# Optimization experiments

Measured on AMD Instinct MI355X. Metric: run time of the kernel, lower is better.

## Reference

```python
import jax, jax.numpy as jnp
import numpy as np

B, D, H, W, T, C = 2, 16, 16, 16, 16, 96
NH = 4                      # num_heads
WS = (4, 4, 4, 4)           # window size
SS = (2, 2, 2, 2)           # shift size
EPS = 1e-5
HIDDEN = 4 * C


def _compute_mask():
    # Standard Swin shifted-window attention mask, extended to 4D.
    img = np.zeros((D, H, W, T), np.float32)
    sl = [[slice(0, -WS[i]), slice(-WS[i], -SS[i]), slice(-SS[i], None)] for i in range(4)]
    cnt = 0
    for a in sl[0]:
        for b in sl[1]:
            for c in sl[2]:
                for d in sl[3]:
                    img[a, b, c, d] = cnt
                    cnt += 1
    x = img.reshape(D // WS[0], WS[0], H // WS[1], WS[1], W // WS[2], WS[2], T // WS[3], WS[3])
    x = x.transpose(0, 2, 4, 6, 1, 3, 5, 7).reshape(-1, WS[0] * WS[1] * WS[2] * WS[3])
    diff = x[:, None, :] - x[:, :, None]
    return np.where(diff != 0, np.float32(-100.0), np.float32(0.0))


def setup_inputs() -> dict:
    key = jax.random.key(0)
    ks = jax.random.split(key, 6)
    w = lambda k, shape: jax.random.normal(k, shape, jnp.float32) * 0.02
    return {
        'x': jax.random.normal(ks[0], (B, D, H, W, T, C), jnp.float32),
        'mask_matrix': jnp.asarray(_compute_mask()),
        'norm1_g': jnp.ones((C,), jnp.float32), 'norm1_b': jnp.zeros((C,), jnp.float32),
        'qkv_w': w(ks[1], (3 * C, C)), 'qkv_b': jnp.zeros((3 * C,), jnp.float32),
        'proj_w': w(ks[2], (C, C)), 'proj_b': jnp.zeros((C,), jnp.float32),
        'norm2_g': jnp.ones((C,), jnp.float32), 'norm2_b': jnp.zeros((C,), jnp.float32),
        'fc1_w': w(ks[3], (HIDDEN, C)), 'fc1_b': jnp.zeros((HIDDEN,), jnp.float32),
        'fc2_w': w(ks[4], (C, HIDDEN)), 'fc2_b': jnp.zeros((C,), jnp.float32),
    }


def _ln(x, g, b):
    mu = jnp.mean(x, -1, keepdims=True)
    var = jnp.var(x, -1, keepdims=True)
    return (x - mu) * jax.lax.rsqrt(var + EPS) * g + b


def _partition(x):
    # (B, D, H, W, T, C) -> (B*nw, N, C)
    b, c = x.shape[0], x.shape[-1]
    x = x.reshape(b, D // WS[0], WS[0], H // WS[1], WS[1], W // WS[2], WS[2], T // WS[3], WS[3], c)
    x = x.transpose(0, 1, 3, 5, 7, 2, 4, 6, 8, 9)
    return x.reshape(-1, WS[0] * WS[1] * WS[2] * WS[3], c)


def _reverse(win, b):
    c = win.shape[-1]
    x = win.reshape(b, D // WS[0], H // WS[1], W // WS[2], T // WS[3], WS[0], WS[1], WS[2], WS[3], c)
    x = x.transpose(0, 1, 5, 2, 6, 3, 7, 4, 8, 9)
    return x.reshape(b, D, H, W, T, c)


def reference(x, mask_matrix, norm1_g, norm1_b, qkv_w, qkv_b, proj_w, proj_b,
              norm2_g, norm2_b, fc1_w, fc1_b, fc2_w, fc2_b):
    b, c = x.shape[0], x.shape[-1]
    hd = c // NH
    scale = hd ** -0.5
    shortcut = x
    # norm -> (no pad needed: dims divisible by window) -> cyclic shift
    xn = _ln(x, norm1_g, norm1_b)
    xs = jnp.roll(xn, shift=(-SS[0], -SS[1], -SS[2], -SS[3]), axis=(1, 2, 3, 4))
    win = _partition(xs)                              # (B_, N, C)
    B_, N, _ = win.shape
    qkv = (win @ qkv_w.T + qkv_b).reshape(B_, N, 3, NH, hd).transpose(2, 0, 3, 1, 4)
    q, k, v = qkv[0] * scale, qkv[1], qkv[2]          # (B_, NH, N, hd)
    attn = jnp.einsum('bhid,bhjd->bhij', q, k)        # (B_, NH, N, N)
    nw = mask_matrix.shape[0]
    attn = attn.reshape(B_ // nw, nw, NH, N, N) + mask_matrix[None, :, None]
    attn = jax.nn.softmax(attn.reshape(B_, NH, N, N), axis=-1)
    out = jnp.einsum('bhij,bhjd->bhid', attn, v)
    out = out.transpose(0, 2, 1, 3).reshape(B_, N, c)
    out = out @ proj_w.T + proj_b
    xr = _reverse(out, b)
    xr = jnp.roll(xr, shift=SS, axis=(1, 2, 3, 4))    # reverse cyclic shift
    x = shortcut + xr
    # MLP block
    h = _ln(x, norm2_g, norm2_b)
    h = jax.nn.gelu(h @ fc1_w.T + fc1_b, approximate=False)
    return x + (h @ fc2_w.T + fc2_b)
```

## Files before the change

### kernel.cpp

```cpp
#include <hip/hip_runtime.h>

#define TOK   131072
#define BWIN  512

typedef __attribute__((ext_vector_type(8))) short bf16x8;
typedef __attribute__((ext_vector_type(4))) short bf16x4;
typedef __attribute__((ext_vector_type(4))) float f32x4;

__device__ __forceinline__ unsigned short f2us(float f) {
  union { float f; unsigned int i; } x; x.f = f;
  return (unsigned short)((x.i + 0x7fffu + ((x.i >> 16) & 1u)) >> 16);
}
__device__ __forceinline__ unsigned cvtpk(float lo, float hi) {
  unsigned r;
  asm("v_cvt_pk_bf16_f32 %0, %1, %2" : "=v"(r) : "v"(lo), "v"(hi));
  return r;
}
union U8 { uint2 u; bf16x4 v; };

#define IW1   0
#define IW2   36864
#define IQKV  73728
#define IPROJ 104448
#define IMG_SHORTS 113664

__global__ __launch_bounds__(256) void k_prepw(
    const float* __restrict__ fc1_w, const float* __restrict__ fc2_w,
    const float* __restrict__ qkv_w, const float* __restrict__ proj_w,
    unsigned short* __restrict__ img) {
  int i = blockIdx.x * 256 + threadIdx.x;
  const int l = (i >> 3) & 63, j = i & 7;
  const int quad = l >> 4, l15 = l & 15;
  float v = 0.f;
  if (i < 36864) {
    int f = i >> 9; int nc = f / 18, rem = f - nc * 18;
    int ks = rem / 6, nt = rem - ks * 6;
    v = fc1_w[(size_t)(nc * 96 + nt * 16 + l15) * 96 + ks * 32 + quad * 8 + j];
  } else if (i < 73728) {
    int f = (i - 36864) >> 9; int nc = f / 18, rem = f - nc * 18;
    int ks = rem / 6, nt = rem - ks * 6;
    v = fc2_w[(size_t)(nt * 16 + l15) * 384 + nc * 96 + ks * 32 + quad * 8 + j];
  } else if (i < 104448) {
    int f = (i - 73728) >> 9; int h = f / 15, rem = f - h * 15;
    int ks = rem / 5, mt = rem - ks * 5;
    int e = mt * 16 + l15;
    if (e < 72) {
      int grp = e / 24, rr = e - grp * 24;
      v = qkv_w[(size_t)(grp * 96 + h * 24 + rr) * 96 + ks * 32 + quad * 8 + j];
    }
  } else {
    int f = (i - 104448) >> 9; int ks = f / 6, nt = f - ks * 6;
    v = proj_w[(size_t)(nt * 16 + l15) * 96 + ks * 32 + quad * 8 + j];
  }
  img[i] = f2us(v);
}

__global__ __launch_bounds__(256) void k_ln1(const float* __restrict__ x,
                                             const float* __restrict__ g,
                                             const float* __restrict__ b,
                                             unsigned short* __restrict__ xn) {
  const int r = threadIdx.x >> 1, hf = threadIdx.x & 1;
  const int t = blockIdx.x * 128 + r;
  const int b_ = t >> 8, n = t & 255;
  const int batch = b_ >> 8, wi = b_ & 255;
  const int wd = (wi >> 6) & 3, wh = (wi >> 4) & 3, ww = (wi >> 2) & 3, wt = wi & 3;
  const int aa = (n >> 6) & 3, bb = (n >> 4) & 3, cc = (n >> 2) & 3, dd = n & 3;
  const int sd = (wd * 4 + aa + 2) & 15, sh = (wh * 4 + bb + 2) & 15;
  const int sw = (ww * 4 + cc + 2) & 15, st = (wt * 4 + dd + 2) & 15;
  const size_t gg = ((((size_t)(batch * 16 + sd) * 16 + sh) * 16 + sw) * 16 + st);

  const float4* base = (const float4*)(x + gg * 96 + hf * 48);
  float v[48];
  float s = 0.f, q2 = 0.f;
  #pragma unroll
  for (int j = 0; j < 12; j++) {
    float4 f = base[j];
    v[4 * j] = f.x; v[4 * j + 1] = f.y; v[4 * j + 2] = f.z; v[4 * j + 3] = f.w;
    s += f.x + f.y + f.z + f.w;
    q2 += f.x * f.x + f.y * f.y + f.z * f.z + f.w * f.w;
  }
  s += __shfl_xor(s, 1); q2 += __shfl_xor(q2, 1);
  const float mu = s * (1.f / 96.f);
  const float var = q2 * (1.f / 96.f) - mu * mu;
  const float rs = rsqrtf(fmaxf(var, 0.f) + 1e-5f);
  unsigned int* row = (unsigned int*)xn + (size_t)t * 48 + hf * 24;
  #pragma unroll
  for (int jj = 0; jj < 24; jj++) {
    int k0 = hf * 48 + 2 * jj;
    float a0 = (v[2 * jj]     - mu) * rs * g[k0]     + b[k0];
    float a1 = (v[2 * jj + 1] - mu) * rs * g[k0 + 1] + b[k0 + 1];
    row[jj] = cvtpk(a0, a1);
  }
}

__global__ __launch_bounds__(256, 2) void k_win(
    const unsigned short* __restrict__ xn,
    const unsigned short* __restrict__ img,
    const float* __restrict__ qkv_b,
    unsigned short* __restrict__ og) {
  __shared__ __align__(16) short s_k[256 * 36];
  __shared__ __align__(16) short s_vt[32 * 260];
  __shared__ unsigned char s_lb[256];

  const int tid = threadIdx.x;
  const int w = tid >> 6, l = tid & 63, quad = l >> 4, l15 = l & 15;
  const int q0 = w * 64;
  const int b_ = blockIdx.x;
  const int wi = b_ & 255;
  const int wd = (wi >> 6) & 3, wh = (wi >> 4) & 3, ww = (wi >> 2) & 3, wt = wi & 3;
  const float scale = 0.20412414523193154f;
  const f32x4 fz = {0.f, 0.f, 0.f, 0.f};

  {
    const int n = tid;
    const int aa = (n >> 6) & 3, bb = (n >> 4) & 3, cc = (n >> 2) & 3, dd = n & 3;
    const int p0 = wd * 4 + aa, p1 = wh * 4 + bb, p2 = ww * 4 + cc, p3 = wt * 4 + dd;
    const int r0 = p0 >= 14 ? 2 : (p0 >= 12 ? 1 : 0);
    const int r1 = p1 >= 14 ? 2 : (p1 >= 12 ? 1 : 0);
    const int r2 = p2 >= 14 ? 2 : (p2 >= 12 ? 1 : 0);
    const int r3 = p3 >= 14 ? 2 : (p3 >= 12 ? 1 : 0);
    s_lb[n] = (unsigned char)(((r0 * 3 + r1) * 3 + r2) * 3 + r3);
    *(uint2*)&s_k[n * 36 + 24] = make_uint2(0u, 0u);
    *(uint2*)&s_k[n * 36 + 28] = make_uint2(0u, 0u);
    unsigned int* vz = (unsigned int*)(s_vt + 24 * 260);
    for (int i = tid; i < 8 * 130; i += 256) vz[i] = 0u;
  }
  __syncthreads();

  const unsigned short* xw = xn + (size_t)b_ * 256 * 96;
  const unsigned short* wq = img + IQKV;

  for (int h = 0; h < 4; h++) {
    f32x4 acc[5][4];
    #pragma unroll
    for (int mt = 0; mt < 5; mt++)
      #pragma unroll
      for (int nt = 0; nt < 4; nt++) acc[mt][nt] = fz;
    #pragma unroll
    for (int ks = 0; ks < 3; ks++) {
      bf16x8 aw[5];
      #pragma unroll
      for (int mt = 0; mt < 5; mt++)
        aw[mt] = *(const bf16x8*)(wq + ((h * 3 + ks) * 5 + mt) * 512 + l * 8);
      #pragma unroll
      for (int nt = 0; nt < 4; nt++) {
        bf16x8 bx = *(const bf16x8*)(xw + (size_t)(q0 + nt * 16 + l15) * 96 + ks * 32 + quad * 8);
        #pragma unroll
        for (int mt = 0; mt < 5; mt++)
          acc[mt][nt] = __builtin_amdgcn_mfma_f32_16x16x32_bf16(aw[mt], bx, acc[mt][nt], 0, 0, 0);
      }
    }
    U8 qq[2][4];
    #pragma unroll
    for (int mt = 0; mt < 2; mt++) {
      const int e0 = mt * 16 + quad * 4;
      float b0 = qkv_b[h * 24 + e0],     b1 = qkv_b[h * 24 + e0 + 1];
      float b2 = qkv_b[h * 24 + e0 + 2], b3 = qkv_b[h * 24 + e0 + 3];
      #pragma unroll
      for (int nt = 0; nt < 4; nt++) {
        qq[mt][nt].u.x = cvtpk((acc[mt][nt][0] + b0) * scale, (acc[mt][nt][1] + b1) * scale);
        qq[mt][nt].u.y = cvtpk((acc[mt][nt][2] + b2) * scale, (acc[mt][nt][3] + b3) * scale);
      }
    }
    #pragma unroll
    for (int mt = 1; mt < 5; mt++) {
      const int e0 = mt * 16 + quad * 4;
      #pragma unroll
      for (int nt = 0; nt < 4; nt++) {
        const int tok = q0 + nt * 16 + l15;
        if (e0 >= 24 && e0 < 48) {
          const int e = e0 - 24;
          uint2 pk;
          pk.x = cvtpk(acc[mt][nt][0] + qkv_b[96 + h * 24 + e],
                       acc[mt][nt][1] + qkv_b[96 + h * 24 + e + 1]);
          pk.y = cvtpk(acc[mt][nt][2] + qkv_b[96 + h * 24 + e + 2],
                       acc[mt][nt][3] + qkv_b[96 + h * 24 + e + 3]);
          *(uint2*)&s_k[tok * 36 + e] = pk;
        } else if (e0 >= 48 && e0 < 72) {
          const int e = e0 - 48;
          #pragma unroll
          for (int r = 0; r < 4; r++)
            s_vt[(e + r) * 260 + tok] = (short)f2us(acc[mt][nt][r] + qkv_b[192 + h * 24 + e + r]);
        }
      }
    }
    __syncthreads();
    #pragma unroll 1
    for (int mt4 = 0; mt4 < 4; mt4++) {
      const int qt0 = q0 + mt4 * 16;
      f32x4 sc[16];
      #pragma unroll
      for (int km = 0; km < 16; km++) sc[km] = fz;
      const bf16x4 bq0 = qq[0][mt4].v, bq1 = qq[1][mt4].v;
      __builtin_amdgcn_s_setprio(1);
      #pragma unroll
      for (int km = 0; km < 16; km++) {
        bf16x4 ak0 = *(const bf16x4*)&s_k[(km * 16 + l15) * 36 + quad * 4];
        bf16x4 ak1 = *(const bf16x4*)&s_k[(km * 16 + l15) * 36 + 16 + quad * 4];
        sc[km] = __builtin_amdgcn_mfma_f32_16x16x16bf16_1k(ak0, bq0, sc[km], 0, 0, 0);
        sc[km] = __builtin_amdgcn_mfma_f32_16x16x16bf16_1k(ak1, bq1, sc[km], 0, 0, 0);
      }
      __builtin_amdgcn_s_setprio(0);
      const unsigned lq = s_lb[qt0 + l15];
      float rsum = 0.f;
      #pragma unroll
      for (int km = 0; km < 16; km++) {
        unsigned lj = *(const unsigned*)&s_lb[km * 16 + quad * 4];
        float p0 = ((lj & 255u)         == lq) ? __expf(sc[km][0]) : 0.f;
        float p1 = (((lj >> 8) & 255u)  == lq) ? __expf(sc[km][1]) : 0.f;
        float p2 = (((lj >> 16) & 255u) == lq) ? __expf(sc[km][2]) : 0.f;
        float p3 = ((lj >> 24)          == lq) ? __expf(sc[km][3]) : 0.f;
        sc[km][0] = p0; sc[km][1] = p1; sc[km][2] = p2; sc[km][3] = p3;
        rsum += (p0 + p1) + (p2 + p3);
      }
      rsum += __shfl_xor(rsum, 16, 64);
      rsum += __shfl_xor(rsum, 32, 64);
      const float inv = 1.f / rsum;
      f32x4 ov0 = fz, ov1 = fz;
      __builtin_amdgcn_s_setprio(1);
      #pragma unroll
      for (int km = 0; km < 16; km++) {
        U8 bp;
        bp.u.x = cvtpk(sc[km][0], sc[km][1]);
        bp.u.y = cvtpk(sc[km][2], sc[km][3]);
        bf16x4 av0 = *(const bf16x4*)&s_vt[l15 * 260 + km * 16 + quad * 4];
        bf16x4 av1 = *(const bf16x4*)&s_vt[(16 + l15) * 260 + km * 16 + quad * 4];
        ov0 = __builtin_amdgcn_mfma_f32_16x16x16bf16_1k(av0, bp.v, ov0, 0, 0, 0);
        ov1 = __builtin_amdgcn_mfma_f32_16x16x16bf16_1k(av1, bp.v, ov1, 0, 0, 0);
      }
      __builtin_amdgcn_s_setprio(0);
      uint2 o0, o1;
      o0.x = cvtpk(ov0[0] * inv, ov0[1] * inv);
      o0.y = cvtpk(ov0[2] * inv, ov0[3] * inv);
      o1.x = cvtpk(ov1[0] * inv, ov1[1] * inv);
      o1.y = cvtpk(ov1[2] * inv, ov1[3] * inv);
      size_t ob = ((size_t)b_ * 256 + qt0 + l15) * 96 + h * 24;
      *(uint2*)&og[ob + quad * 4] = o0;
      if (quad < 2) *(uint2*)&og[ob + 16 + quad * 4] = o1;
    }
    __syncthreads();
  }
}

__global__ __launch_bounds__(256, 2) void k_proj(
    const unsigned short* __restrict__ og, const float* __restrict__ x,
    const unsigned short* __restrict__ img,
    const float* __restrict__ proj_b, float* __restrict__ out) {
  const int tid = threadIdx.x;
  const int w = tid >> 6, l = tid & 63, quad = l >> 4, l15 = l & 15;
  const int t0 = blockIdx.x * 128;
  const f32x4 fz = {0.f, 0.f, 0.f, 0.f};

  f32x4 acc[2][6];
  #pragma unroll
  for (int m = 0; m < 2; m++)
    #pragma unroll
    for (int nt = 0; nt < 6; nt++) acc[m][nt] = fz;

  #pragma unroll
  for (int ks = 0; ks < 3; ks++) {
    bf16x8 bw[6];
    #pragma unroll
    for (int nt = 0; nt < 6; nt++)
      bw[nt] = *(const bf16x8*)(img + IPROJ + (ks * 6 + nt) * 512 + l * 8);
    #pragma unroll
    for (int m = 0; m < 2; m++) {
      bf16x8 af = *(const bf16x8*)(og + (size_t)(t0 + w * 32 + m * 16 + l15) * 96 + ks * 32 + quad * 8);
      #pragma unroll
      for (int nt = 0; nt < 6; nt++)
        acc[m][nt] = __builtin_amdgcn_mfma_f32_16x16x32_bf16(af, bw[nt], acc[m][nt], 0, 0, 0);
    }
  }

  #pragma unroll
  for (int m = 0; m < 2; m++) {
    #pragma unroll
    for (int r = 0; r < 4; r++) {
      const int T = t0 + w * 32 + m * 16 + quad * 4 + r;
      const int b_ = T >> 8, n = T & 255;
      const int batch = b_ >> 8, wi = b_ & 255;
      const int wd = (wi >> 6) & 3, wh = (wi >> 4) & 3, ww = (wi >> 2) & 3, wt = wi & 3;
      const int aa = (n >> 6) & 3, bb = (n >> 4) & 3, cc = (n >> 2) & 3, dd = n & 3;
      const int sd = (wd * 4 + aa + 2) & 15, sh = (wh * 4 + bb + 2) & 15;
      const int sw = (ww * 4 + cc + 2) & 15, st = (wt * 4 + dd + 2) & 15;
      const size_t gg = ((((size_t)(batch * 16 + sd) * 16 + sh) * 16 + sw) * 16 + st);
      #pragma unroll
      for (int nt = 0; nt < 6; nt++) {
        int c = nt * 16 + l15;
        out[gg * 96 + c] = x[gg * 96 + c] + proj_b[c] + acc[m][nt][r];
      }
    }
  }
}

__global__ __launch_bounds__(256, 3) void k_mlp(
    float* __restrict__ io,
    const float* __restrict__ n2g, const float* __restrict__ n2b,
    const unsigned short* __restrict__ img,
    const float* __restrict__ fc1_b, const float* __restrict__ fc2_b) {
  __shared__ __align__(16) short s_a[128 * 104];
  __shared__ __align__(16) short s_h[128 * 104];

  const int tid = threadIdx.x;
  const int w = tid >> 6, l = tid & 63;
  const int quad = l >> 4, l15 = l & 15;
  const size_t t0 = (size_t)blockIdx.x * 128;
  const f32x4 fz = {0.f, 0.f, 0.f, 0.f};

  {
    const int r = tid >> 1, hf = tid & 1;
    const float4* base = (const float4*)(io + (t0 + r) * 96 + hf * 48);
    float v[48];
    float s = 0.f, q = 0.f;
    #pragma unroll
    for (int j = 0; j < 12; j++) {
      float4 f = base[j];
      v[4 * j] = f.x; v[4 * j + 1] = f.y; v[4 * j + 2] = f.z; v[4 * j + 3] = f.w;
      s += f.x + f.y + f.z + f.w;
      q += f.x * f.x + f.y * f.y + f.z * f.z + f.w * f.w;
    }
    s += __shfl_xor(s, 1); q += __shfl_xor(q, 1);
    const float mu = s * (1.f / 96.f);
    const float var = q * (1.f / 96.f) - mu * mu;
    const float rs = rsqrtf(fmaxf(var, 0.f) + 1e-5f);
    unsigned int* row = (unsigned int*)&s_a[r * 104] + hf * 24;
    #pragma unroll
    for (int jj = 0; jj < 24; jj++) {
      int k0 = hf * 48 + 2 * jj;
      float lo = (v[2 * jj]     - mu) * rs * n2g[k0]     + n2b[k0];
      float hi = (v[2 * jj + 1] - mu) * rs * n2g[k0 + 1] + n2b[k0 + 1];
      row[jj] = cvtpk(lo, hi);
    }
  }

  f32x4 acc2[2][6];
  #pragma unroll
  for (int m = 0; m < 2; m++)
    #pragma unroll
    for (int i = 0; i < 6; i++) acc2[m][i] = fz;

  for (int nc = 0; nc < 4; nc++) {
    f32x4 acc1[2][6];
    #pragma unroll
    for (int m = 0; m < 2; m++)
      #pragma unroll
      for (int i = 0; i < 6; i++) acc1[m][i] = fz;
    #pragma unroll
    for (int ks = 0; ks < 3; ks++) {
      bf16x8 bw[6];
      #pragma unroll
      for (int nt = 0; nt < 6; nt++)
        bw[nt] = *(const bf16x8*)(img + IW1 + ((nc * 3 + ks) * 6 + nt) * 512 + l * 8);
      #pragma unroll
      for (int m = 0; m < 2; m++) {
        bf16x8 af = *(const bf16x8*)&s_a[(w * 32 + m * 16 + l15) * 104 + ks * 32 + quad * 8];
        #pragma unroll
        for (int nt = 0; nt < 6; nt++)
          acc1[m][nt] = __builtin_amdgcn_mfma_f32_16x16x32_bf16(af, bw[nt], acc1[m][nt], 0, 0, 0);
      }
    }
    #pragma unroll
    for (int m = 0; m < 2; m++)
      #pragma unroll
      for (int nt = 0; nt < 6; nt++) {
        int col = nt * 16 + l15;
        float bv = fc1_b[nc * 96 + col];
        #pragma unroll
        for (int r = 0; r < 4; r++) {
          float z = acc1[m][nt][r] + bv;
          float g = 0.5f * z * (1.f + erff(z * 0.70710678118654752f));
          s_h[(w * 32 + m * 16 + quad * 4 + r) * 104 + col] = (short)f2us(g);
        }
      }
    #pragma unroll
    for (int ks = 0; ks < 3; ks++) {
      bf16x8 bw[6];
      #pragma unroll
      for (int nt = 0; nt < 6; nt++)
        bw[nt] = *(const bf16x8*)(img + IW2 + ((nc * 3 + ks) * 6 + nt) * 512 + l * 8);
      #pragma unroll
      for (int m = 0; m < 2; m++) {
        bf16x8 af = *(const bf16x8*)&s_h[(w * 32 + m * 16 + l15) * 104 + ks * 32 + quad * 8];
        #pragma unroll
        for (int nt = 0; nt < 6; nt++)
          acc2[m][nt] = __builtin_amdgcn_mfma_f32_16x16x32_bf16(af, bw[nt], acc2[m][nt], 0, 0, 0);
      }
    }
  }

  #pragma unroll
  for (int m = 0; m < 2; m++)
    #pragma unroll
    for (int nt = 0; nt < 6; nt++) {
      int col = nt * 16 + l15;
      float bv = fc2_b[col];
      #pragma unroll
      for (int r = 0; r < 4; r++) {
        size_t idx = (t0 + w * 32 + m * 16 + quad * 4 + r) * 96 + col;
        io[idx] = io[idx] + acc2[m][nt][r] + bv;
      }
    }
}

extern "C" void kernel_launch(void* const* d_in, const int* in_sizes, int n_in,
                              void* d_out, int out_size, void* d_ws, size_t ws_size,
                              hipStream_t stream) {
  const float* x      = (const float*)d_in[0];
  const float* n1g    = (const float*)d_in[2];
  const float* n1b    = (const float*)d_in[3];
  const float* qkv_w  = (const float*)d_in[4];
  const float* qkv_b  = (const float*)d_in[5];
  const float* proj_w = (const float*)d_in[6];
  const float* proj_b = (const float*)d_in[7];
  const float* n2g    = (const float*)d_in[8];
  const float* n2b    = (const float*)d_in[9];
  const float* fc1_w  = (const float*)d_in[10];
  const float* fc1_b  = (const float*)d_in[11];
  const float* fc2_w  = (const float*)d_in[12];
  const float* fc2_b  = (const float*)d_in[13];
  float* out = (float*)d_out;

  char* ws = (char*)d_ws;
  unsigned short* xn  = (unsigned short*)ws;
  unsigned short* img = (unsigned short*)(ws + 25165824u);
  unsigned short* og  = (unsigned short*)(ws + 25165824u + 227328u);

  k_prepw<<<IMG_SHORTS / 256, 256, 0, stream>>>(fc1_w, fc2_w, qkv_w, proj_w, img);
  k_ln1<<<TOK / 128, 256, 0, stream>>>(x, n1g, n1b, xn);
  k_win<<<BWIN, 256, 0, stream>>>(xn, img, qkv_b, og);
  k_proj<<<TOK / 128, 256, 0, stream>>>(og, x, img, proj_b, out);
  k_mlp<<<TOK / 128, 256, 0, stream>>>(out, n2g, n2b, img, fc1_b, fc2_b);
}
```

Before: 314.8 us.

## Fuse projection, residual, LayerNorm2 and MLP into one kernel

Merges k_proj and k_mlp into a single kernel. The projection result plus residual stays in registers, LayerNorm2 is computed with cross-lane shuffles, and the MLP output is scattered straight to its final un-shifted location. This removes one fp32 write and re-read of the full 50MB intermediate plus one launch. In exchange it raises register pressure (x2, gg and pacc held across the MLP) while keeping launch bounds at 2 blocks per SM instead of 3, which may lower occupancy. The final stores are scattered rather than contiguous.

```diff
diff --git a/kernel.cpp b/kernel.cpp
--- a/kernel.cpp
+++ b/kernel.cpp
@@ -242,21 +242,33 @@
   }
 }
 
-__global__ __launch_bounds__(256, 2) void k_proj(
+__global__ __launch_bounds__(256, 2) void k_pm(
     const unsigned short* __restrict__ og, const float* __restrict__ x,
     const unsigned short* __restrict__ img,
-    const float* __restrict__ proj_b, float* __restrict__ out) {
+    const float* __restrict__ proj_b,
+    const float* __restrict__ n2g, const float* __restrict__ n2b,
+    const float* __restrict__ fc1_b, const float* __restrict__ fc2_b,
+    float* __restrict__ out) {
+  __shared__ __align__(16) short s_a[128 * 104];
+  __shared__ __align__(16) short s_h[128 * 104];
+
   const int tid = threadIdx.x;
   const int w = tid >> 6, l = tid & 63, quad = l >> 4, l15 = l & 15;
   const int t0 = blockIdx.x * 128;
   const f32x4 fz = {0.f, 0.f, 0.f, 0.f};
 
-  f32x4 acc[2][6];
+  float gn[6], bn[6], pb[6], f2[6];
+  #pragma unroll
+  for (int nt = 0; nt < 6; nt++) {
+    int c = nt * 16 + l15;
+    gn[nt] = n2g[c]; bn[nt] = n2b[c]; pb[nt] = proj_b[c]; f2[nt] = fc2_b[c];
+  }
+
+  f32x4 pacc[2][6];
   #pragma unroll
   for (int m = 0; m < 2; m++)
     #pragma unroll
-    for (int nt = 0; nt < 6; nt++) acc[m][nt] = fz;
-
+    for (int nt = 0; nt < 6; nt++) pacc[m][nt] = fz;
   #pragma unroll
   for (int ks = 0; ks < 3; ks++) {
     bf16x8 bw[6];
@@ -268,10 +280,12 @@
       bf16x8 af = *(const bf16x8*)(og + (size_t)(t0 + w * 32 + m * 16 + l15) * 96 + ks * 32 + quad * 8);
       #pragma unroll
       for (int nt = 0; nt < 6; nt++)
-        acc[m][nt] = __builtin_amdgcn_mfma_f32_16x16x32_bf16(af, bw[nt], acc[m][nt], 0, 0, 0);
-    }
-  }
-
+        pacc[m][nt] = __builtin_amdgcn_mfma_f32_16x16x32_bf16(af, bw[nt], pacc[m][nt], 0, 0, 0);
+    }
+  }
+
+  float x2[2][6][4];
+  size_t gg[2][4];
   #pragma unroll
   for (int m = 0; m < 2; m++) {
     #pragma unroll
@@ -283,53 +297,26 @@
       const int aa = (n >> 6) & 3, bb = (n >> 4) & 3, cc = (n >> 2) & 3, dd = n & 3;
       const int sd = (wd * 4 + aa + 2) & 15, sh = (wh * 4 + bb + 2) & 15;
       const int sw = (ww * 4 + cc + 2) & 15, st = (wt * 4 + dd + 2) & 15;
-      const size_t gg = ((((size_t)(batch * 16 + sd) * 16 + sh) * 16 + sw) * 16 + st);
+      gg[m][r] = ((((size_t)(batch * 16 + sd) * 16 + sh) * 16 + sw) * 16 + st);
+      float s = 0.f, q = 0.f;
       #pragma unroll
       for (int nt = 0; nt < 6; nt++) {
-        int c = nt * 16 + l15;
-        out[gg * 96 + c] = x[gg * 96 + c] + proj_b[c] + acc[m][nt][r];
-      }
-    }
-  }
-}
-
-__global__ __launch_bounds__(256, 3) void k_mlp(
-    float* __restrict__ io,
-    const float* __restrict__ n2g, const float* __restrict__ n2b,
-    const unsigned short* __restrict__ img,
-    const float* __restrict__ fc1_b, const float* __restrict__ fc2_b) {
-  __shared__ __align__(16) short s_a[128 * 104];
-  __shared__ __align__(16) short s_h[128 * 104];
-
-  const int tid = threadIdx.x;
-  const int w = tid >> 6, l = tid & 63;
-  const int quad = l >> 4, l15 = l & 15;
-  const size_t t0 = (size_t)blockIdx.x * 128;
-  const f32x4 fz = {0.f, 0.f, 0.f, 0.f};
-
-  {
-    const int r = tid >> 1, hf = tid & 1;
-    const float4* base = (const float4*)(io + (t0 + r) * 96 + hf * 48);
-    float v[48];
-    float s = 0.f, q = 0.f;
-    #pragma unroll
-    for (int j = 0; j < 12; j++) {
-      float4 f = base[j];
-      v[4 * j] = f.x; v[4 * j + 1] = f.y; v[4 * j + 2] = f.z; v[4 * j + 3] = f.w;
-      s += f.x + f.y + f.z + f.w;
-      q += f.x * f.x + f.y * f.y + f.z * f.z + f.w * f.w;
-    }
-    s += __shfl_xor(s, 1); q += __shfl_xor(q, 1);
-    const float mu = s * (1.f / 96.f);
-    const float var = q * (1.f / 96.f) - mu * mu;
-    const float rs = rsqrtf(fmaxf(var, 0.f) + 1e-5f);
-    unsigned int* row = (unsigned int*)&s_a[r * 104] + hf * 24;
-    #pragma unroll
-    for (int jj = 0; jj < 24; jj++) {
-      int k0 = hf * 48 + 2 * jj;
-      float lo = (v[2 * jj]     - mu) * rs * n2g[k0]     + n2b[k0];
-      float hi = (v[2 * jj + 1] - mu) * rs * n2g[k0 + 1] + n2b[k0 + 1];
-      row[jj] = cvtpk(lo, hi);
+        float v = x[gg[m][r] * 96 + nt * 16 + l15] + pb[nt] + pacc[m][nt][r];
+        x2[m][nt][r] = v;
+        s += v; q += v * v;
+      }
+      s += __shfl_xor(s, 1); q += __shfl_xor(q, 1);
+      s += __shfl_xor(s, 2); q += __shfl_xor(q, 2);
+      s += __shfl_xor(s, 4); q += __shfl_xor(q, 4);
+      s += __shfl_xor(s, 8); q += __shfl_xor(q, 8);
+      const float mu = s * (1.f / 96.f);
+      const float var = q * (1.f / 96.f) - mu * mu;
+      const float rs = rsqrtf(fmaxf(var, 0.f) + 1e-5f);
+      const int tr = w * 32 + m * 16 + quad * 4 + r;
+      #pragma unroll
+      for (int nt = 0; nt < 6; nt++)
+        s_a[tr * 104 + nt * 16 + l15] =
+            (short)f2us((x2[m][nt][r] - mu) * rs * gn[nt] + bn[nt]);
     }
   }
 
@@ -391,15 +378,10 @@
   #pragma unroll
   for (int m = 0; m < 2; m++)
     #pragma unroll
-    for (int nt = 0; nt < 6; nt++) {
-      int col = nt * 16 + l15;
-      float bv = fc2_b[col];
-      #pragma unroll
-      for (int r = 0; r < 4; r++) {
-        size_t idx = (t0 + w * 32 + m * 16 + quad * 4 + r) * 96 + col;
-        io[idx] = io[idx] + acc2[m][nt][r] + bv;
-      }
-    }
+    for (int r = 0; r < 4; r++)
+      #pragma unroll
+      for (int nt = 0; nt < 6; nt++)
+        out[gg[m][r] * 96 + nt * 16 + l15] = x2[m][nt][r] + acc2[m][nt][r] + f2[nt];
 }
 
 extern "C" void kernel_launch(void* const* d_in, const int* in_sizes, int n_in,
@@ -428,6 +410,5 @@
   k_prepw<<<IMG_SHORTS / 256, 256, 0, stream>>>(fc1_w, fc2_w, qkv_w, proj_w, img);
   k_ln1<<<TOK / 128, 256, 0, stream>>>(x, n1g, n1b, xn);
   k_win<<<BWIN, 256, 0, stream>>>(xn, img, qkv_b, og);
-  k_proj<<<TOK / 128, 256, 0, stream>>>(og, x, img, proj_b, out);
-  k_mlp<<<TOK / 128, 256, 0, stream>>>(out, n2g, n2b, img, fc1_b, fc2_b);
-}
+  k_pm<<<TOK / 128, 256, 0, stream>>>(og, x, img, proj_b, n2g, n2b, fc1_b, fc2_b, out);
+}
```

Result: faster. 299.3 us (-4.9%).
